# Optimization experiments

Hardware: AMD Instinct MI355X
Metric: run time of the kernel (lower is better)

The kernel has to match this reference:

```python
import jax, jax.numpy as jnp
import numpy as np

N = 50000      # num nodes
E = 800000     # num edges per edge set (before self loops)
F_IN = 256     # encoding_size
F_EMB = 256    # embedding_size
PE = 98        # d2an positional features (beijing)
ALPHA1 = 0.5
ALPHA2 = 0.5


def _uniform_linear(key, out_f, in_f):
    # torch.nn.Linear default init: U(-1/sqrt(in_f), 1/sqrt(in_f))
    s = 1.0 / np.sqrt(in_f)
    return jax.random.uniform(key, (out_f, in_f), jnp.float32, -s, s)


def setup_inputs() -> dict:
    key = jax.random.key(0)
    ks = jax.random.split(key, 18)
    inp = {
        'x': jax.random.normal(ks[0], (N, F_IN), jnp.float32),
        'd2an': jax.random.normal(ks[1], (N, PE), jnp.float32),
        'edge_index_l0': jax.random.randint(ks[2], (2, E), 0, N, jnp.int32),
        'edge_attr_l0': jax.random.uniform(ks[3], (E,), jnp.float32),
        'edge_index_l1': jax.random.randint(ks[4], (2, E), 0, N, jnp.int32),
        'edge_attr_l1': jax.random.uniform(ks[5], (E,), jnp.float32),
        # nodeLin of conv1/conv2 (used only on firstLayer with usePE)
        'Wnode1': _uniform_linear(ks[6], F_IN, F_IN + PE),
        'Wnode2': _uniform_linear(ks[7], F_IN, F_IN + PE),
        # lin1/lin2 of each conv layer (bias-free linears)
        'W11': _uniform_linear(ks[8], F_EMB, F_IN),
        'W12': _uniform_linear(ks[9], F_EMB, F_IN),
        'W21': _uniform_linear(ks[10], F_EMB, F_IN),
        'W22': _uniform_linear(ks[11], F_EMB, F_IN),
        'W31': _uniform_linear(ks[12], F_EMB, F_EMB),
        'W32': _uniform_linear(ks[13], F_EMB, F_EMB),
        'W41': _uniform_linear(ks[14], F_EMB, F_EMB),
        'W42': _uniform_linear(ks[15], F_EMB, F_EMB),
    }
    return inp


def _pos_knn_gnn_layer(x, row, col, attr, d2an, Wnode, W1, W2, first):
    """PosKnnGNNLayer.forward with useSI=True, usePE=True (eval mode).

    message = deg_norm * (x_j @ W1.T) + edge_norm * (x_j @ W2.T), scatter-add to col.
    Linearity lets us aggregate (norm * x_j) first, then apply W1/W2 once per node.
    """
    n = x.shape[0]
    loop = jnp.arange(n, dtype=row.dtype)
    row = jnp.concatenate([row, loop])          # source j
    col = jnp.concatenate([col, loop])          # target i
    attr = jnp.concatenate([attr, jnp.ones((n,), attr.dtype)])  # self-loop weight 1.0

    if first:
        x = jnp.concatenate([x, d2an], axis=1) @ Wnode.T  # [n, F_IN]

    deg = jax.ops.segment_sum(jnp.ones_like(attr), col, num_segments=n)
    dinv = jnp.where(deg > 0, deg ** -0.5, 0.0)
    deg_norm = dinv[row] * dinv[col]            # [E']

    einv = jnp.where(attr > 0, attr ** -0.5, 0.0)
    edge_norm = jnp.minimum(einv, 1.0)          # clamp values > 1.0 to 1.0

    xj = x[row]                                  # gather [E', F]
    a1 = jax.ops.segment_sum(deg_norm[:, None] * xj, col, num_segments=n)
    a2 = jax.ops.segment_sum(edge_norm[:, None] * xj, col, num_segments=n)
    return a1 @ W1.T + a2 @ W2.T                 # [n, F_EMB]


def reference(x, d2an, edge_index_l0, edge_attr_l0, edge_index_l1, edge_attr_l1,
              Wnode1, Wnode2, W11, W12, W21, W22, W31, W32, W41, W42):
    r0, c0 = edge_index_l0[0], edge_index_l0[1]
    r1, c1 = edge_index_l1[0], edge_index_l1[1]

    x0 = jax.nn.relu(_pos_knn_gnn_layer(x, r0, c0, edge_attr_l0, d2an, Wnode1, W11, W12, True))
    x1 = jax.nn.relu(_pos_knn_gnn_layer(x, r1, c1, edge_attr_l1, d2an, Wnode2, W21, W22, True))
    h = ALPHA1 * x0 + ALPHA2 * x1               # dropout p=0.3 is identity in eval

    x0 = jax.nn.relu(_pos_knn_gnn_layer(h, r0, c0, edge_attr_l0, None, None, W31, W32, False))
    x1 = jax.nn.relu(_pos_knn_gnn_layer(h, r1, c1, edge_attr_l1, None, None, W41, W42, False))
    return ALPHA1 * x0 + ALPHA2 * x1
```

## Files before the change

kernel.cpp:

```cpp
#include <hip/hip_runtime.h>


using bf16x8  = __attribute__((ext_vector_type(8))) __bf16;
using floatx4 = __attribute__((ext_vector_type(4))) float;
using f32x2   = __attribute__((ext_vector_type(2))) float;

__device__ __forceinline__ float b2f(unsigned short b) {
    return __uint_as_float(((unsigned)b) << 16);
}
__device__ __forceinline__ unsigned short f2b(float f) {
    unsigned u = __float_as_uint(f);
    return (unsigned short)((u + 0x7FFFu + ((u >> 16) & 1u)) >> 16);
}
__device__ __forceinline__ unsigned short f2h(float f) {
    _Float16 h = (_Float16)f;
    return __builtin_bit_cast(unsigned short, h);
}
__device__ __forceinline__ float h2f(unsigned short u) {
    return (float)__builtin_bit_cast(_Float16, u);
}

__global__ void k_front(
    const int* __restrict__ col0, const int* __restrict__ col1, int E,
    int* __restrict__ cnt0, int* __restrict__ cnt1,
    const float* __restrict__ x, const float* __restrict__ pe,
    unsigned short* __restrict__ xc,
    const float* __restrict__ Wn1, const float* __restrict__ Wn2,
    const float* __restrict__ W11, const float* __restrict__ W12,
    const float* __restrict__ W21, const float* __restrict__ W22,
    const float* __restrict__ W31, const float* __restrict__ W32,
    const float* __restrict__ W41, const float* __restrict__ W42,
    unsigned short* __restrict__ wn0c, unsigned short* __restrict__ wn1c,
    unsigned short* __restrict__ wc0, unsigned short* __restrict__ wc1,
    unsigned short* __restrict__ wc2, unsigned short* __restrict__ wc3,
    int n, int F, int PEd, int KC, int KP) {
    int idx = blockIdx.x * 256 + threadIdx.x;
    if (idx < E) { atomicAdd(&cnt0[col0[idx]], 1); return; }
    idx -= E;
    if (idx < E) { atomicAdd(&cnt1[col1[idx]], 1); return; }
    idx -= E;
    const int CH = KP >> 3;
    const int NXC = n * CH;
    if (idx < NXC) {
        int i = idx / CH, c = idx - i * CH;
        int k = c << 3;
        uint4 o;
        if (k + 8 <= F) {
            const float4* px = (const float4*)(x + (size_t)i * F + k);
            float4 v0 = px[0];
            float4 v1 = px[1];
            o.x = (unsigned)f2b(v0.x) | ((unsigned)f2b(v0.y) << 16);
            o.y = (unsigned)f2b(v0.z) | ((unsigned)f2b(v0.w) << 16);
            o.z = (unsigned)f2b(v1.x) | ((unsigned)f2b(v1.y) << 16);
            o.w = (unsigned)f2b(v1.z) | ((unsigned)f2b(v1.w) << 16);
        } else if (k < KC) {
            const float* pp = pe + (size_t)i * PEd + (k - F);
            int rem = KC - k;
            float e0 = pp[0];
            float e1 = (1 < rem) ? pp[1] : 0.f;
            float e2 = (2 < rem) ? pp[2] : 0.f;
            float e3 = (3 < rem) ? pp[3] : 0.f;
            float e4 = (4 < rem) ? pp[4] : 0.f;
            float e5 = (5 < rem) ? pp[5] : 0.f;
            float e6 = (6 < rem) ? pp[6] : 0.f;
            float e7 = (7 < rem) ? pp[7] : 0.f;
            o.x = (unsigned)f2b(e0) | ((unsigned)f2b(e1) << 16);
            o.y = (unsigned)f2b(e2) | ((unsigned)f2b(e3) << 16);
            o.z = (unsigned)f2b(e4) | ((unsigned)f2b(e5) << 16);
            o.w = (unsigned)f2b(e6) | ((unsigned)f2b(e7) << 16);
        } else {
            o.x = o.y = o.z = o.w = 0u;
        }
        *(uint4*)(xc + (size_t)idx * 8) = o;
        return;
    }
    idx -= NXC;
    int npad = F * KP;
    if (idx < 2 * npad) {
        const float* W = (idx < npad) ? Wn1 : Wn2;
        unsigned short* Wc = (idx < npad) ? wn0c : wn1c;
        int t = (idx < npad) ? idx : idx - npad;
        int o = t / KP, k = t - o * KP;
        Wc[t] = f2b(k < KC ? W[(size_t)o * KC + k] : 0.0f);
        return;
    }
    int t = idx - 2 * npad;
    int seg = F * 512;
    if (t >= 4 * seg) return;
    int which = t / seg;
    int r = t - which * seg;
    const float* Wa = (which == 0) ? W11 : (which == 1) ? W21 : (which == 2) ? W31 : W41;
    const float* Wb = (which == 0) ? W12 : (which == 1) ? W22 : (which == 2) ? W32 : W42;
    unsigned short* Wc = (which == 0) ? wc0 : (which == 1) ? wc1 : (which == 2) ? wc2 : wc3;
    int o = r >> 9, k = r & 511;
    float v = (k < 256) ? Wa[(size_t)o * 256 + k] : Wb[(size_t)o * 256 + (k - 256)];
    Wc[r] = f2b(v);
}

__global__ void k_alloc(
    const int* __restrict__ cnt0, const int* __restrict__ cnt1,
    int* __restrict__ tot,
    int* __restrict__ off0, int* __restrict__ off1,
    float* __restrict__ dinv0, float* __restrict__ dinv1,
    int* __restrict__ cur0, int* __restrict__ cur1, int n) {
    int i = blockIdx.x * 256 + threadIdx.x;
    if (i >= n) return;
    const int* cnt = blockIdx.y ? cnt1 : cnt0;
    int* off = blockIdx.y ? off1 : off0;
    float* dinv = blockIdx.y ? dinv1 : dinv0;
    int* cur = blockIdx.y ? cur1 : cur0;
    int ci = cnt[i];
    int pad = (ci + 4) & ~3;
    int o = atomicAdd(&tot[blockIdx.y], pad);
    off[i] = o;
    cur[i] = o;
    dinv[i] = rsqrtf((float)(ci + 1));
}

__global__ void k_fillpad(
    const int* __restrict__ ei0, const float* __restrict__ ea0,
    const int* __restrict__ ei1, const float* __restrict__ ea1,
    int E, int EB,
    const int* __restrict__ cnt0, const int* __restrict__ cnt1,
    const int* __restrict__ off0, const int* __restrict__ off1,
    const float* __restrict__ dinv0, const float* __restrict__ dinv1,
    int* __restrict__ cur0, int* __restrict__ cur1,
    uint2* __restrict__ rec0, uint2* __restrict__ rec1, int n) {
    const int s = blockIdx.y;
    const float* dinv = s ? dinv1 : dinv0;
    uint2* rec = s ? rec1 : rec0;
    int t = blockIdx.x * 256 + threadIdx.x;
    if (t < EB) {
        int e = t;
        if (e >= E) return;
        const int* ei = s ? ei1 : ei0;
        const float* ea = s ? ea1 : ea0;
        int* cur = s ? cur1 : cur0;
        int r = ei[e];
        int c = ei[E + e];
        float a = ea[e];
        float w2 = (a > 0.0f) ? fminf(rsqrtf(a), 1.0f) : 0.0f;
        float w1 = dinv[r] * dinv[c];
        int p = atomicAdd(&cur[c], 1);
        rec[p] = make_uint2((unsigned)r,
                            ((unsigned)f2h(w1) << 16) | (unsigned)f2h(w2));
    } else {
        int i = t - EB;
        if (i >= n) return;
        const int* cnt = s ? cnt1 : cnt0;
        const int* off = s ? off1 : off0;
        int ci = cnt[i];
        int p = off[i] + ci, pe = off[i] + ((ci + 4) & ~3);
        float di = dinv[i];
        rec[p++] = make_uint2((unsigned)i,
                              ((unsigned)f2h(di * di) << 16) | 0x3C00u);
        for (; p < pe; ++p) rec[p] = make_uint2(0u, 0u);
    }
}


#define AGG4(g, wsel)                                                         \
    do {                                                                      \
        float w1 = h2f((unsigned short)((wsel) >> 16));                       \
        float w2 = h2f((unsigned short)((wsel) & 0xFFFFu));                   \
        f32x2 w1v = {w1, w1};                                                 \
        f32x2 w2v = {w2, w2};                                                 \
        f32x2 v;                                                              \
        v.x = __uint_as_float((g).x << 16);                                   \
        v.y = __uint_as_float((g).x & 0xFFFF0000u);                           \
        c1a = __builtin_elementwise_fma(w1v, v, c1a);                         \
        c2a = __builtin_elementwise_fma(w2v, v, c2a);                         \
        v.x = __uint_as_float((g).y << 16);                                   \
        v.y = __uint_as_float((g).y & 0xFFFF0000u);                           \
        c1b = __builtin_elementwise_fma(w1v, v, c1b);                         \
        c2b = __builtin_elementwise_fma(w2v, v, c2b);                         \
    } while (0)

__global__ __launch_bounds__(256) void k_agg(
    const unsigned short* __restrict__ X0, const unsigned short* __restrict__ X1,
    const int* __restrict__ cnt0, const int* __restrict__ cnt1,
    const int* __restrict__ off0, const int* __restrict__ off1,
    const uint2* __restrict__ rec0, const uint2* __restrict__ rec1,
    unsigned short* __restrict__ A0, unsigned short* __restrict__ A1, int n) {
    const int s = blockIdx.y;
    const unsigned short* X = s ? X1 : X0;
    const int* cnt = s ? cnt1 : cnt0;
    const int* off = s ? off1 : off0;
    const uint2* rec = s ? rec1 : rec0;
    unsigned short* A = s ? A1 : A0;

    const int gw = (blockIdx.x * 256 + threadIdx.x) >> 6;
    const int lane = threadIdx.x & 63;
    if (gw >= n) return;

    const int e0 = __builtin_amdgcn_readfirstlane(off[gw]);
    const int cv = __builtin_amdgcn_readfirstlane(cnt[gw]);
    const uint2* X2 = (const uint2*)X;

    f32x2 c1a = {0.f, 0.f}, c1b = {0.f, 0.f};
    f32x2 c2a = {0.f, 0.f}, c2b = {0.f, 0.f};

    const uint4* recq = (const uint4*)(rec + e0);
    const int nit = ((cv + 4) & ~3) >> 2;
    #pragma unroll 2
    for (int it = 0; it < nit; ++it) {
        uint4 qa = recq[it * 2];
        uint4 qb = recq[it * 2 + 1];
        unsigned s0 = (unsigned)__builtin_amdgcn_readfirstlane(qa.x);
        unsigned s1 = (unsigned)__builtin_amdgcn_readfirstlane(qa.z);
        unsigned s2 = (unsigned)__builtin_amdgcn_readfirstlane(qb.x);
        unsigned s3 = (unsigned)__builtin_amdgcn_readfirstlane(qb.z);
        uint2 g0 = X2[(size_t)s0 * 64 + lane];
        uint2 g1 = X2[(size_t)s1 * 64 + lane];
        uint2 g2 = X2[(size_t)s2 * 64 + lane];
        uint2 g3 = X2[(size_t)s3 * 64 + lane];
        AGG4(g0, qa.y);
        AGG4(g1, qa.w);
        AGG4(g2, qb.y);
        AGG4(g3, qb.w);
    }

    uint2 o1, o2;
    o1.x = (unsigned)f2b(c1a.x) | ((unsigned)f2b(c1a.y) << 16);
    o1.y = (unsigned)f2b(c1b.x) | ((unsigned)f2b(c1b.y) << 16);
    o2.x = (unsigned)f2b(c2a.x) | ((unsigned)f2b(c2a.y) << 16);
    o2.y = (unsigned)f2b(c2b.x) | ((unsigned)f2b(c2b.y) << 16);
    *(uint2*)(A + (size_t)gw * 512 + lane * 4) = o1;
    *(uint2*)(A + (size_t)gw * 512 + 256 + lane * 4) = o2;
}

#define GLL(g, l) \
    __builtin_amdgcn_global_load_lds((__attribute__((address_space(1))) void*)(g), \
                                     (__attribute__((address_space(3))) void*)(l), 16, 0, 0)

__global__ __launch_bounds__(256, 3) void gemm_bt(
    const unsigned short* __restrict__ A,
    const unsigned short* __restrict__ B0, const unsigned short* __restrict__ B1,
    int M, int K, int Nc,
    unsigned short* __restrict__ outH0, unsigned short* __restrict__ outH1) {
    const unsigned short* B = blockIdx.y ? B1 : B0;
    unsigned short* outH = blockIdx.y ? outH1 : outH0;

    __shared__ __align__(16) unsigned short sA[128 * 32];
    __shared__ __align__(16) unsigned short sB[128 * 32];
    const int tid = threadIdx.x;
    const int lane = tid & 63;
    const int wave = tid >> 6;
    const int bm = blockIdx.z * 128;
    const int bn = blockIdx.x * 128;

    const int r0 = wave * 32 + (lane >> 2);
    const int kcol = (lane & 3) * 8;
    const int ga0 = min(bm + r0, M - 1);
    const int ga1 = min(bm + r0 + 16, M - 1);
    const int gb0 = min(bn + r0, Nc - 1);
    const int gb1 = min(bn + r0 + 16, Nc - 1);
    const unsigned short* pa0 = A + (size_t)ga0 * K + kcol;
    const unsigned short* pa1 = A + (size_t)ga1 * K + kcol;
    const unsigned short* pb0 = B + (size_t)gb0 * K + kcol;
    const unsigned short* pb1 = B + (size_t)gb1 * K + kcol;
    unsigned short* la0 = &sA[wave * 1024];
    unsigned short* la1 = &sA[wave * 1024 + 512];
    unsigned short* lb0 = &sB[wave * 1024];
    unsigned short* lb1 = &sB[wave * 1024 + 512];

    floatx4 acc[4][4];
    #pragma unroll
    for (int i = 0; i < 4; i++)
        #pragma unroll
        for (int j = 0; j < 4; j++) acc[i][j] = (floatx4){0.f, 0.f, 0.f, 0.f};

    const int mbase = (wave & 1) * 64 + (lane & 15);
    const int nbase = (wave >> 1) * 64 + (lane & 15);
    const int koff = (lane >> 4) * 8;

    for (int kk = 0; kk < K; kk += 32) {
        GLL(pa0 + kk, la0);
        GLL(pa1 + kk, la1);
        GLL(pb0 + kk, lb0);
        GLL(pb1 + kk, lb1);
        __syncthreads();
        bf16x8 af[4], bf[4];
        #pragma unroll
        for (int mi = 0; mi < 4; mi++)
            af[mi] = *(const bf16x8*)&sA[(mbase + mi * 16) * 32 + koff];
        #pragma unroll
        for (int ni = 0; ni < 4; ni++)
            bf[ni] = *(const bf16x8*)&sB[(nbase + ni * 16) * 32 + koff];
        #pragma unroll
        for (int mi = 0; mi < 4; mi++)
            #pragma unroll
            for (int ni = 0; ni < 4; ni++)
                acc[mi][ni] = __builtin_amdgcn_mfma_f32_16x16x32_bf16(
                    af[mi], bf[ni], acc[mi][ni], 0, 0, 0);
        __syncthreads();
    }

    const int crow = bm + (wave & 1) * 64 + (lane >> 4) * 4;
    const int ccol = bn + (wave >> 1) * 64 + (lane & 15);
    #pragma unroll
    for (int mi = 0; mi < 4; mi++)
        #pragma unroll
        for (int ni = 0; ni < 4; ni++)
            #pragma unroll
            for (int r = 0; r < 4; r++) {
                int row = crow + mi * 16 + r;
                if (row >= M) continue;
                int col = ccol + ni * 16;
                outH[(size_t)row * Nc + col] = f2b(acc[mi][ni][r]);
            }
}

__global__ __launch_bounds__(256, 3) void gemm_dual(
    const unsigned short* __restrict__ A0, const unsigned short* __restrict__ B0,
    const unsigned short* __restrict__ A1, const unsigned short* __restrict__ B1,
    int M, int K, int Nc,
    float* __restrict__ outF, unsigned short* __restrict__ outH, float alpha) {
    __shared__ __align__(16) unsigned short sA[128 * 32];
    __shared__ __align__(16) unsigned short sB[128 * 32];
    const int tid = threadIdx.x;
    const int lane = tid & 63;
    const int wave = tid >> 6;
    const int bm = blockIdx.y * 128;
    const int bn = blockIdx.x * 128;

    const int r0 = wave * 32 + (lane >> 2);
    const int kcol = (lane & 3) * 8;
    const int ga0 = min(bm + r0, M - 1);
    const int ga1 = min(bm + r0 + 16, M - 1);
    const int gb0 = min(bn + r0, Nc - 1);
    const int gb1 = min(bn + r0 + 16, Nc - 1);
    unsigned short* la0 = &sA[wave * 1024];
    unsigned short* la1 = &sA[wave * 1024 + 512];
    unsigned short* lb0 = &sB[wave * 1024];
    unsigned short* lb1 = &sB[wave * 1024 + 512];

    const int mbase = (wave & 1) * 64 + (lane & 15);
    const int nbase = (wave >> 1) * 64 + (lane & 15);
    const int koff = (lane >> 4) * 8;

    floatx4 acc[4][4];
    uint2 resp[4][4];

    #pragma unroll
    for (int pass = 0; pass < 2; pass++) {
        const unsigned short* A = pass ? A1 : A0;
        const unsigned short* B = pass ? B1 : B0;
        const unsigned short* pa0 = A + (size_t)ga0 * K + kcol;
        const unsigned short* pa1 = A + (size_t)ga1 * K + kcol;
        const unsigned short* pb0 = B + (size_t)gb0 * K + kcol;
        const unsigned short* pb1 = B + (size_t)gb1 * K + kcol;
        #pragma unroll
        for (int i = 0; i < 4; i++)
            #pragma unroll
            for (int j = 0; j < 4; j++) acc[i][j] = (floatx4){0.f, 0.f, 0.f, 0.f};

        for (int kk = 0; kk < K; kk += 32) {
            GLL(pa0 + kk, la0);
            GLL(pa1 + kk, la1);
            GLL(pb0 + kk, lb0);
            GLL(pb1 + kk, lb1);
            __syncthreads();
            bf16x8 af[4], bf[4];
            #pragma unroll
            for (int mi = 0; mi < 4; mi++)
                af[mi] = *(const bf16x8*)&sA[(mbase + mi * 16) * 32 + koff];
            #pragma unroll
            for (int ni = 0; ni < 4; ni++)
                bf[ni] = *(const bf16x8*)&sB[(nbase + ni * 16) * 32 + koff];
            #pragma unroll
            for (int mi = 0; mi < 4; mi++)
                #pragma unroll
                for (int ni = 0; ni < 4; ni++)
                    acc[mi][ni] = __builtin_amdgcn_mfma_f32_16x16x32_bf16(
                        af[mi], bf[ni], acc[mi][ni], 0, 0, 0);
            __syncthreads();
        }
        if (pass == 0) {
            #pragma unroll
            for (int mi = 0; mi < 4; mi++)
                #pragma unroll
                for (int ni = 0; ni < 4; ni++) {
                    float r0f = fmaxf(acc[mi][ni][0], 0.0f);
                    float r1f = fmaxf(acc[mi][ni][1], 0.0f);
                    float r2f = fmaxf(acc[mi][ni][2], 0.0f);
                    float r3f = fmaxf(acc[mi][ni][3], 0.0f);
                    resp[mi][ni].x = (unsigned)f2b(r0f) | ((unsigned)f2b(r1f) << 16);
                    resp[mi][ni].y = (unsigned)f2b(r2f) | ((unsigned)f2b(r3f) << 16);
                }
        }
    }

    const int crow = bm + (wave & 1) * 64 + (lane >> 4) * 4;
    const int ccol = bn + (wave >> 1) * 64 + (lane & 15);
    #pragma unroll
    for (int mi = 0; mi < 4; mi++)
        #pragma unroll
        for (int ni = 0; ni < 4; ni++) {
            float p0 = b2f((unsigned short)(resp[mi][ni].x & 0xFFFFu));
            float p1 = b2f((unsigned short)(resp[mi][ni].x >> 16));
            float p2 = b2f((unsigned short)(resp[mi][ni].y & 0xFFFFu));
            float p3 = b2f((unsigned short)(resp[mi][ni].y >> 16));
            #pragma unroll
            for (int r = 0; r < 4; r++) {
                int row = crow + mi * 16 + r;
                if (row >= M) continue;
                int col = ccol + ni * 16;
                float pr = (r == 0) ? p0 : (r == 1) ? p1 : (r == 2) ? p2 : p3;
                float v = alpha * (pr + fmaxf(acc[mi][ni][r], 0.0f));
                size_t idx = (size_t)row * Nc + col;
                if (outF) outF[idx] = v;
                else      outH[idx] = f2b(v);
            }
        }
}


extern "C" void kernel_launch(void* const* d_in, const int* in_sizes, int n_in,
                              void* d_out, int out_size, void* d_ws, size_t ws_size,
                              hipStream_t stream) {
    const int F = 256;
    const int N = in_sizes[0] / F;
    const int PEd = in_sizes[1] / N;
    const int E = in_sizes[2] / 2;
    const int KC = F + PEd;
    const int KP = (KC + 31) & ~31;

    const float* x   = (const float*)d_in[0];
    const float* pe  = (const float*)d_in[1];
    const int*   ei0 = (const int*)d_in[2];
    const float* ea0 = (const float*)d_in[3];
    const int*   ei1 = (const int*)d_in[4];
    const float* ea1 = (const float*)d_in[5];
    const float* Wn1 = (const float*)d_in[6];
    const float* Wn2 = (const float*)d_in[7];
    const float* W11 = (const float*)d_in[8];
    const float* W12 = (const float*)d_in[9];
    const float* W21 = (const float*)d_in[10];
    const float* W22 = (const float*)d_in[11];
    const float* W31 = (const float*)d_in[12];
    const float* W32 = (const float*)d_in[13];
    const float* W41 = (const float*)d_in[14];
    const float* W42 = (const float*)d_in[15];
    float* out = (float*)d_out;

    char* p = (char*)d_ws;
    auto alloc = [&](size_t b) -> char* {
        char* r = p;
        p += (b + 255) & ~(size_t)255;
        return r;
    };
    int*   cnt0  = (int*)alloc((size_t)N * 4);
    int*   cnt1  = (int*)alloc((size_t)N * 4);
    int*   tot   = (int*)alloc(2 * 4);
    int*   off0  = (int*)alloc((size_t)N * 4);
    int*   off1  = (int*)alloc((size_t)N * 4);
    int*   cur0  = (int*)alloc((size_t)N * 4);
    int*   cur1  = (int*)alloc((size_t)N * 4);
    float* dinv0 = (float*)alloc((size_t)N * 4);
    float* dinv1 = (float*)alloc((size_t)N * 4);
    uint2* rec0  = (uint2*)alloc(((size_t)E + 4ull * N) * 8);
    uint2* rec1  = (uint2*)alloc(((size_t)E + 4ull * N) * 8);
    unsigned short* wn0c = (unsigned short*)alloc((size_t)F * KP * 2);
    unsigned short* wn1c = (unsigned short*)alloc((size_t)F * KP * 2);
    unsigned short* wc0  = (unsigned short*)alloc((size_t)F * 512 * 2);
    unsigned short* wc1  = (unsigned short*)alloc((size_t)F * 512 * 2);
    unsigned short* wc2  = (unsigned short*)alloc((size_t)F * 512 * 2);
    unsigned short* wc3  = (unsigned short*)alloc((size_t)F * 512 * 2);
    unsigned short* xa   = (unsigned short*)alloc((size_t)N * 512 * 2);
    unsigned short* xb   = xa + (size_t)N * 256;
    unsigned short* h    = (unsigned short*)alloc((size_t)N * F * 2);
    unsigned short* a12  = (unsigned short*)alloc((size_t)N * 512 * 2);
    unsigned short* xc   = a12;
    unsigned short* a12bL1 = (unsigned short*)d_out;
    unsigned short* a12bL2 = xa;

    const int B = 256;
    const int gE = (E + B - 1) / B;
    const int gN = (N + B - 1) / B;
    const int gW = (N + 3) / 4;
    const int Mb = (N + 127) / 128;
    dim3 dual_grid(2, Mb);
    dim3 bt_grid(2, 2, Mb);

    hipMemsetAsync(cnt0, 0, (size_t)((char*)off0 - (char*)cnt0), stream);
    {
        const int NXC = N * (KP >> 3);
        const int TOTW = 2 * F * KP + 4 * F * 512;
        long long totThreads = 2ll * E + NXC + TOTW;
        k_front<<<(unsigned)((totThreads + B - 1) / B), B, 0, stream>>>(
            ei0 + E, ei1 + E, E, cnt0, cnt1, x, pe, xc,
            Wn1, Wn2, W11, W12, W21, W22, W31, W32, W41, W42,
            wn0c, wn1c, wc0, wc1, wc2, wc3, N, F, PEd, KC, KP);
    }

    k_alloc<<<dim3(gN, 2), B, 0, stream>>>(cnt0, cnt1, tot, off0, off1,
                                           dinv0, dinv1, cur0, cur1, N);
    k_fillpad<<<dim3(gE + gN, 2), B, 0, stream>>>(
        ei0, ea0, ei1, ea1, E, gE * B, cnt0, cnt1, off0, off1,
        dinv0, dinv1, cur0, cur1, rec0, rec1, N);

    gemm_bt<<<bt_grid, B, 0, stream>>>(xc, wn0c, wn1c, N, KP, F, xa, xb);

    k_agg<<<dim3(gW, 2), B, 0, stream>>>(xa, xb, cnt0, cnt1, off0, off1,
                                         rec0, rec1, a12, a12bL1, N);
    gemm_dual<<<dual_grid, B, 0, stream>>>(a12, wc0, a12bL1, wc1, N, 512, F,
                                           nullptr, h, 0.5f);

    k_agg<<<dim3(gW, 2), B, 0, stream>>>(h, h, cnt0, cnt1, off0, off1,
                                         rec0, rec1, a12, a12bL2, N);
    gemm_dual<<<dual_grid, B, 0, stream>>>(a12, wc2, a12bL2, wc3, N, 512, F,
                                           out, nullptr, 0.5f);
}
```

Before: 707.7 us.

## Split aggregation into feature slices with eight nodes per wave

Reworks the CSR gather-aggregate kernel. Each wave now handles eight destination nodes, with eight lanes per node covering one 64-byte feature slice, and the grid is split into eight feature slices. Before, one wave walked one node's full 512-byte row in groups of four edges. Per-lane edge iteration with __any-based loop exit replaces the padded groups of four, so the fill kernel no longer writes zero padding records. The aim is better L2 locality per slice and less padding work. The cost is divergence from unequal degrees within a wave and eight re-reads of the edge records.

```diff
diff --git a/kernel.cpp b/kernel.cpp
--- a/kernel.cpp
+++ b/kernel.cpp
@@ -150,83 +150,75 @@
         const int* cnt = s ? cnt1 : cnt0;
         const int* off = s ? off1 : off0;
         int ci = cnt[i];
-        int p = off[i] + ci, pe = off[i] + ((ci + 4) & ~3);
         float di = dinv[i];
-        rec[p++] = make_uint2((unsigned)i,
+        rec[off[i] + ci] = make_uint2((unsigned)i,
                               ((unsigned)f2h(di * di) << 16) | 0x3C00u);
-        for (; p < pe; ++p) rec[p] = make_uint2(0u, 0u);
-    }
-}
-
-
-#define AGG4(g, wsel)                                                         \
-    do {                                                                      \
-        float w1 = h2f((unsigned short)((wsel) >> 16));                       \
-        float w2 = h2f((unsigned short)((wsel) & 0xFFFFu));                   \
-        f32x2 w1v = {w1, w1};                                                 \
-        f32x2 w2v = {w2, w2};                                                 \
-        f32x2 v;                                                              \
-        v.x = __uint_as_float((g).x << 16);                                   \
-        v.y = __uint_as_float((g).x & 0xFFFF0000u);                           \
-        c1a = __builtin_elementwise_fma(w1v, v, c1a);                         \
-        c2a = __builtin_elementwise_fma(w2v, v, c2a);                         \
-        v.x = __uint_as_float((g).y << 16);                                   \
-        v.y = __uint_as_float((g).y & 0xFFFF0000u);                           \
-        c1b = __builtin_elementwise_fma(w1v, v, c1b);                         \
-        c2b = __builtin_elementwise_fma(w2v, v, c2b);                         \
-    } while (0)
+    }
+}
 
 __global__ __launch_bounds__(256) void k_agg(
     const unsigned short* __restrict__ X0, const unsigned short* __restrict__ X1,
     const int* __restrict__ cnt0, const int* __restrict__ cnt1,
     const int* __restrict__ off0, const int* __restrict__ off1,
     const uint2* __restrict__ rec0, const uint2* __restrict__ rec1,
-    unsigned short* __restrict__ A0, unsigned short* __restrict__ A1, int n) {
-    const int s = blockIdx.y;
-    const unsigned short* X = s ? X1 : X0;
-    const int* cnt = s ? cnt1 : cnt0;
-    const int* off = s ? off1 : off0;
-    const uint2* rec = s ? rec1 : rec0;
-    unsigned short* A = s ? A1 : A0;
-
-    const int gw = (blockIdx.x * 256 + threadIdx.x) >> 6;
+    unsigned short* __restrict__ A0, unsigned short* __restrict__ A1,
+    int n, int GN) {
+    const int bid = blockIdx.x;
+    const int slice = bid & 7;
+    const int t = bid >> 3;
+    const int set = (t >= GN) ? 1 : 0;
+    const int g = t - set * GN;
+
+    const char* Xb = (const char*)(set ? X1 : X0);
+    const int* cnt = set ? cnt1 : cnt0;
+    const int* off = set ? off1 : off0;
+    const uint2* rec = set ? rec1 : rec0;
+    unsigned short* A = set ? A1 : A0;
+
+    const int wave = threadIdx.x >> 6;
     const int lane = threadIdx.x & 63;
-    if (gw >= n) return;
-
-    const int e0 = __builtin_amdgcn_readfirstlane(off[gw]);
-    const int cv = __builtin_amdgcn_readfirstlane(cnt[gw]);
-    const uint2* X2 = (const uint2*)X;
+    const int nd = (g * 4 + wave) * 8 + (lane >> 3);
+    const int c = lane & 7;
+    const bool live = nd < n;
+    const int ndc = live ? nd : 0;
+
+    const int offn = off[ndc];
+    const int lim = live ? (cnt[ndc] + 1) : 0;
+
+    const unsigned soff = (unsigned)slice * 64 + (unsigned)c * 8;
 
     f32x2 c1a = {0.f, 0.f}, c1b = {0.f, 0.f};
     f32x2 c2a = {0.f, 0.f}, c2b = {0.f, 0.f};
 
-    const uint4* recq = (const uint4*)(rec + e0);
-    const int nit = ((cv + 4) & ~3) >> 2;
-    #pragma unroll 2
-    for (int it = 0; it < nit; ++it) {
-        uint4 qa = recq[it * 2];
-        uint4 qb = recq[it * 2 + 1];
-        unsigned s0 = (unsigned)__builtin_amdgcn_readfirstlane(qa.x);
-        unsigned s1 = (unsigned)__builtin_amdgcn_readfirstlane(qa.z);
-        unsigned s2 = (unsigned)__builtin_amdgcn_readfirstlane(qb.x);
-        unsigned s3 = (unsigned)__builtin_amdgcn_readfirstlane(qb.z);
-        uint2 g0 = X2[(size_t)s0 * 64 + lane];
-        uint2 g1 = X2[(size_t)s1 * 64 + lane];
-        uint2 g2 = X2[(size_t)s2 * 64 + lane];
-        uint2 g3 = X2[(size_t)s3 * 64 + lane];
-        AGG4(g0, qa.y);
-        AGG4(g1, qa.w);
-        AGG4(g2, qb.y);
-        AGG4(g3, qb.w);
-    }
-
+    for (int it = 0; ; ++it) {
+        bool valid = it < lim;
+        if (!__any(valid)) break;
+        int ridx = offn + (valid ? it : 0);
+        uint2 q = rec[ridx];
+        unsigned wsel = valid ? q.y : 0u;
+        uint2 gv = *(const uint2*)(Xb + (((size_t)q.x << 9) | soff));
+        float w1 = h2f((unsigned short)(wsel >> 16));
+        float w2 = h2f((unsigned short)(wsel & 0xFFFFu));
+        f32x2 w1v = {w1, w1}, w2v = {w2, w2};
+        f32x2 v0, v1;
+        v0.x = __uint_as_float(gv.x << 16);
+        v0.y = __uint_as_float(gv.x & 0xFFFF0000u);
+        v1.x = __uint_as_float(gv.y << 16);
+        v1.y = __uint_as_float(gv.y & 0xFFFF0000u);
+        c1a = __builtin_elementwise_fma(w1v, v0, c1a);
+        c1b = __builtin_elementwise_fma(w1v, v1, c1b);
+        c2a = __builtin_elementwise_fma(w2v, v0, c2a);
+        c2b = __builtin_elementwise_fma(w2v, v1, c2b);
+    }
+
+    if (!live) return;
     uint2 o1, o2;
     o1.x = (unsigned)f2b(c1a.x) | ((unsigned)f2b(c1a.y) << 16);
     o1.y = (unsigned)f2b(c1b.x) | ((unsigned)f2b(c1b.y) << 16);
     o2.x = (unsigned)f2b(c2a.x) | ((unsigned)f2b(c2a.y) << 16);
     o2.y = (unsigned)f2b(c2b.x) | ((unsigned)f2b(c2b.y) << 16);
-    *(uint2*)(A + (size_t)gw * 512 + lane * 4) = o1;
-    *(uint2*)(A + (size_t)gw * 512 + 256 + lane * 4) = o2;
+    *(uint2*)(A + (size_t)nd * 512 + slice * 32 + c * 4) = o1;
+    *(uint2*)(A + (size_t)nd * 512 + 256 + slice * 32 + c * 4) = o2;
 }
 
 #define GLL(g, l) \
@@ -478,7 +470,8 @@
     const int B = 256;
     const int gE = (E + B - 1) / B;
     const int gN = (N + B - 1) / B;
-    const int gW = (N + 3) / 4;
+    const int GN = (N + 31) / 32;
+    const int NB = 2 * 8 * GN;
     const int Mb = (N + 127) / 128;
     dim3 dual_grid(2, Mb);
     dim3 bt_grid(2, 2, Mb);
@@ -502,13 +495,13 @@
 
     gemm_bt<<<bt_grid, B, 0, stream>>>(xc, wn0c, wn1c, N, KP, F, xa, xb);
 
-    k_agg<<<dim3(gW, 2), B, 0, stream>>>(xa, xb, cnt0, cnt1, off0, off1,
-                                         rec0, rec1, a12, a12bL1, N);
+    k_agg<<<NB, B, 0, stream>>>(xa, xb, cnt0, cnt1, off0, off1,
+                                rec0, rec1, a12, a12bL1, N, GN);
     gemm_dual<<<dual_grid, B, 0, stream>>>(a12, wc0, a12bL1, wc1, N, 512, F,
                                            nullptr, h, 0.5f);
 
-    k_agg<<<dim3(gW, 2), B, 0, stream>>>(h, h, cnt0, cnt1, off0, off1,
-                                         rec0, rec1, a12, a12bL2, N);
+    k_agg<<<NB, B, 0, stream>>>(h, h, cnt0, cnt1, off0, off1,
+                                rec0, rec1, a12, a12bL2, N, GN);
     gemm_dual<<<dual_grid, B, 0, stream>>>(a12, wc2, a12bL2, wc3, N, 512, F,
                                            out, nullptr, 0.5f);
 }
```

Measured after the change: 970.9 us. 37.2% more time.
